# Kernel tuning notes

Measured on AMD Instinct MI355X. Metric: run time of the kernel, lower is better.

The kernel has to match this reference:

```python
import jax, jax.numpy as jnp
import numpy as np

LN_EPS = 1e-5


def _ln(x, g, b):
    m = jnp.mean(x, axis=-1, keepdims=True)
    v = jnp.mean((x - m) ** 2, axis=-1, keepdims=True)
    return (x - m) / jnp.sqrt(v + LN_EPS) * g + b


def setup_inputs() -> dict:
    key = jax.random.key(0)
    ks = jax.random.split(key, 8)
    B, N, S, D, T = 16, 64, 2048, 1024, 768

    def xavier(k, shape):
        fan_in, fan_out = shape
        lim = (6.0 / (fan_in + fan_out)) ** 0.5
        return jax.random.uniform(k, shape, minval=-lim, maxval=lim, dtype=jnp.float32)

    return {
        "prev_states": jax.random.normal(ks[0], (B, N, D), dtype=jnp.float32),
        "input_tokens": jax.random.normal(ks[1], (B, S, T), dtype=jnp.float32),
        # input_projection (token_dim -> state_dim)
        "W_proj": xavier(ks[2], (T, D)),
        "b_proj": jnp.zeros((D,), jnp.float32),
        # three LayerNorms
        "g_state": jnp.ones((D,), jnp.float32), "beta_state": jnp.zeros((D,), jnp.float32),
        "g_input": jnp.ones((D,), jnp.float32), "beta_input": jnp.zeros((D,), jnp.float32),
        "g_out": jnp.ones((D,), jnp.float32), "beta_out": jnp.zeros((D,), jnp.float32),
        # GRU gates (2D -> D); update-gate bias initialized to -1 as in the module
        "W_u": xavier(ks[3], (2 * D, D)), "b_u": jnp.full((D,), -1.0, jnp.float32),
        "W_r": xavier(ks[4], (2 * D, D)), "b_r": jnp.zeros((D,), jnp.float32),
        "W_n": xavier(ks[5], (2 * D, D)), "b_n": jnp.zeros((D,), jnp.float32),
    }


def reference(prev_states, input_tokens, W_proj, b_proj,
              g_state, beta_state, g_input, beta_input, g_out, beta_out,
              W_u, b_u, W_r, b_r, W_n, b_n):
    D = prev_states.shape[-1]
    # project tokens to state dim: (B,S,D)
    tok = input_tokens @ W_proj + b_proj
    # attention routing (routing_weights=None path)
    scores = jnp.einsum('bnd,bsd->bns', prev_states, tok) / jnp.sqrt(jnp.float32(D))
    attn = jax.nn.softmax(scores, axis=-1)
    routed = jnp.einsum('bns,bsd->bnd', attn, tok)  # (B,N,D)
    # GRU-style gated update, vectorized over the num_states axis
    ps_n = _ln(prev_states, g_state, beta_state)
    in_n = _ln(routed, g_input, beta_input)
    concat = jnp.concatenate([ps_n, in_n], axis=-1)  # (B,N,2D)
    u = jax.nn.sigmoid(concat @ W_u + b_u)
    r = jax.nn.sigmoid(concat @ W_r + b_r)
    reset_in = jnp.concatenate([r * ps_n, in_n], axis=-1)
    cand = jnp.tanh(reset_in @ W_n + b_n)  # dropout is identity in eval
    new_state = (1.0 - u) * prev_states + u * cand
    return _ln(new_state, g_out, beta_out)
```

## Files before the change

kernel.cpp:

```cpp
#include <hip/hip_runtime.h>
#include <stdint.h>

typedef __attribute__((ext_vector_type(4))) float floatx4;
typedef __attribute__((ext_vector_type(8))) short shortx8;

#define LN_EPS 1e-5f

__device__ __forceinline__ unsigned short f2b(float f) {
  unsigned u = __builtin_bit_cast(unsigned, f);
  u = (u + 0x7FFFu + ((u >> 16) & 1u)) >> 16;
  return (unsigned short)u;
}
__device__ __forceinline__ float b2f(unsigned short h) {
  return __builtin_bit_cast(float, (unsigned)h << 16);
}

__device__ __forceinline__ void g2l16(const unsigned short* g, unsigned short* l) {
  __builtin_amdgcn_global_load_lds(
      (const __attribute__((address_space(1))) unsigned int*)g,
      (__attribute__((address_space(3))) unsigned int*)l, 16, 0, 0);
}

__device__ __forceinline__ float wave_sum(float v) {
#pragma unroll
  for (int o = 32; o; o >>= 1) v += __shfl_down(v, o, 64);
  return v;
}
__device__ __forceinline__ float block_sum(float v, float* s) {
  v = wave_sum(v);
  __syncthreads();
  if ((threadIdx.x & 63) == 0) s[threadIdx.x >> 6] = v;
  __syncthreads();
  return s[0] + s[1] + s[2] + s[3];
}

__global__ __launch_bounds__(256) void k_transpose_to_bf16(
    const float* __restrict__ in, unsigned short* __restrict__ out, int K, int N) {
  __shared__ float tile[32][33];
  const int k0 = blockIdx.x * 32, n0 = blockIdx.y * 32;
  const int tx = threadIdx.x & 31, ty = threadIdx.x >> 5;
#pragma unroll
  for (int i = 0; i < 32; i += 8)
    tile[ty + i][tx] = in[(long)(k0 + ty + i) * N + n0 + tx];
  __syncthreads();
#pragma unroll
  for (int i = 0; i < 32; i += 8)
    out[(long)(n0 + ty + i) * K + k0 + tx] = f2b(tile[tx][ty + i]);
}

__global__ __launch_bounds__(256) void k_transpose3(
    const float* __restrict__ Wu, const float* __restrict__ Wr,
    const float* __restrict__ Wn, unsigned short* __restrict__ Wtur,
    unsigned short* __restrict__ Wtn) {
  __shared__ float tile[32][33];
  const int which = blockIdx.z;
  const float* in = which == 0 ? Wu : (which == 1 ? Wr : Wn);
  unsigned short* out = which == 0 ? Wtur : (which == 1 ? Wtur + 1024 * 2048 : Wtn);
  const int K = 2048, N = 1024;
  const int k0 = blockIdx.x * 32, n0 = blockIdx.y * 32;
  const int tx = threadIdx.x & 31, ty = threadIdx.x >> 5;
#pragma unroll
  for (int i = 0; i < 32; i += 8)
    tile[ty + i][tx] = in[(long)(k0 + ty + i) * N + n0 + tx];
  __syncthreads();
#pragma unroll
  for (int i = 0; i < 32; i += 8)
    out[(long)(n0 + ty + i) * K + k0 + tx] = f2b(tile[tx][ty + i]);
}

__global__ __launch_bounds__(256) void k_cvt3(
    const float* __restrict__ prev, unsigned short* __restrict__ psb,
    const float* __restrict__ toks, unsigned short* __restrict__ tokb,
    const float* __restrict__ wp, unsigned short* __restrict__ wpb) {
  const long chunk = (long)blockIdx.x * 256 + threadIdx.x;
  const float* src;
  unsigned short* dst;
  long i;
  if (chunk < 262144) { src = prev; dst = psb; i = chunk * 4; }
  else if (chunk < 6553600) { src = toks; dst = tokb; i = (chunk - 262144) * 4; }
  else { src = wp; dst = wpb; i = (chunk - 6553600) * 4; }
  floatx4 v = *(const floatx4*)(src + i);
  unsigned short t4[4];
#pragma unroll
  for (int j = 0; j < 4; j++) t4[j] = f2b(v[j]);
  *(uint2*)(dst + i) = *(uint2*)t4;
}

__global__ __launch_bounds__(256) void k_gemm64(
    const unsigned short* __restrict__ A, long sAb, long sAk, int lda,
    const unsigned short* __restrict__ Bt, long sBb, long sBk, int ldb,
    int K, int nsplit,
    const float* __restrict__ bias, const float* __restrict__ bias2,
    float scale, int mode,
    void* __restrict__ out, int ldc, long sCb, long sCk,
    unsigned short* __restrict__ out2,
    const unsigned short* __restrict__ aux_psn,
    const float* __restrict__ aux_u, const float* __restrict__ aux_prev) {
  __shared__ unsigned short As[64 * 64];
  __shared__ unsigned short Bs[64 * 64];
  const int tid = threadIdx.x;
  const int wave = tid >> 6, lane = tid & 63;
  const int z = blockIdx.z;
  const int b = (nsplit == 2) ? (z >> 1) : z;
  const int kc = (nsplit == 2) ? (z & 1) : 0;
  const int m0 = blockIdx.x * 64, n0 = blockIdx.y * 64;
  const int wm = wave & 1, wn = wave >> 1;
  const int l16 = lane & 15, quad = lane >> 4;
  const int srow8 = lane >> 3;
  const int c8 = ((lane & 7) ^ srow8) * 8;
  const unsigned short* Ab = A + (long)b * sAb + (long)kc * sAk;
  const unsigned short* Bb = Bt + (long)b * sBb + (long)kc * sBk;

  const unsigned short* gA[2];
  const unsigned short* gB[2];
  unsigned short* lA[2];
  unsigned short* lB[2];
#pragma unroll
  for (int j = 0; j < 2; j++) {
    const int rb = wave * 16 + j * 8;
    gA[j] = Ab + (long)(m0 + rb + srow8) * lda + c8;
    gB[j] = Bb + (long)(n0 + rb + srow8) * ldb + c8;
    lA[j] = &As[rb * 64];
    lB[j] = &Bs[rb * 64];
  }
  int offA[2][2], offB[2][2];
#pragma unroll
  for (int ks = 0; ks < 2; ks++)
#pragma unroll
    for (int i = 0; i < 2; i++) {
      int r = wm * 32 + i * 16 + l16;
      offA[ks][i] = r * 64 + (((ks * 4 + quad) ^ (r & 7)) * 8);
      r = wn * 32 + i * 16 + l16;
      offB[ks][i] = r * 64 + (((ks * 4 + quad) ^ (r & 7)) * 8);
    }

  floatx4 acc[2][2] = {};

  for (int k0 = 0; k0 < K; k0 += 64) {
#pragma unroll
    for (int j = 0; j < 2; j++) {
      g2l16(gA[j] + k0, lA[j]);
      g2l16(gB[j] + k0, lB[j]);
    }
    __syncthreads();
#pragma unroll
    for (int ks = 0; ks < 2; ks++) {
      shortx8 af[2], bf[2];
#pragma unroll
      for (int i = 0; i < 2; i++) af[i] = *(const shortx8*)&As[offA[ks][i]];
#pragma unroll
      for (int j = 0; j < 2; j++) bf[j] = *(const shortx8*)&Bs[offB[ks][j]];
#pragma unroll
      for (int i = 0; i < 2; i++)
#pragma unroll
        for (int j = 0; j < 2; j++)
          acc[i][j] = __builtin_amdgcn_mfma_f32_16x16x32_bf16(af[i], bf[j], acc[i][j], 0, 0, 0);
    }
    __syncthreads();
  }

#pragma unroll
  for (int i = 0; i < 2; i++)
#pragma unroll
    for (int j = 0; j < 2; j++) {
      const int rbase = m0 + wm * 32 + i * 16 + quad * 4;
      const int c = n0 + wn * 32 + j * 16 + l16;
      float bval = 0.0f;
      if (bias) bval = (mode == 5 && c >= 1024) ? bias2[c - 1024] : bias[c];
#pragma unroll
      for (int r = 0; r < 4; r++) {
        const int row = rbase + r;
        float v = acc[i][j][r] * scale + bval;
        const long cidx = (long)b * sCb + (long)kc * sCk + (long)row * ldc + c;
        if (mode == 0) {
          out2[cidx] = f2b(expf(v));
        } else if (mode == 1) {
          out2[cidx] = f2b(v);
        } else if (mode == 3) {
          float cand = tanhf(v);
          float u = aux_u[(long)row * 1024 + c];
          float p = aux_prev[(long)row * 1024 + c];
          ((float*)out)[cidx] = (1.0f - u) * p + u * cand;
        } else if (mode == 6) {
          ((float*)out)[cidx] = v + aux_u[row] * bias2[c];
        } else {
          if (c < 1024) {
            ((float*)out)[(long)row * 1024 + c] = 1.0f / (1.0f + expf(-v));
          } else {
            const int cc = c - 1024;
            float rr = 1.0f / (1.0f + expf(-v));
            out2[(long)row * 2048 + cc] = f2b(rr * b2f(aux_psn[(long)row * 2048 + cc]));
          }
        }
      }
    }
}

__global__ __launch_bounds__(256) void k_routed_mfma(
    const unsigned short* __restrict__ attnb,
    const unsigned short* __restrict__ tok,
    float* __restrict__ parts) {
  __shared__ unsigned short As[64 * 40];
  __shared__ unsigned short Bs[32 * 66];
  const int kc = blockIdx.x, nt = blockIdx.y, b = blockIdx.z;
  const int tid = threadIdx.x;
  const int wave = tid >> 6, lane = tid & 63;
  const int wm = wave & 1, wn = wave >> 1;
  const int l16 = lane & 15, quad = lane >> 4;
  const int n0 = nt * 64;
  const long abase = (long)b * 131072 + (long)kc * 1024;
  const long tbase = ((long)b * 2048 + (long)kc * 1024) * 768;
  const int srow = tid >> 2, skc = (tid & 3) * 8;
  const int bk = tid >> 3, bd = (tid & 7) * 8;

  floatx4 acc[2][2] = {};

  for (int k0 = 0; k0 < 1024; k0 += 32) {
    *(uint4*)&As[srow * 40 + skc] =
        *(const uint4*)(attnb + abase + (long)srow * 2048 + k0 + skc);
    {
      uint4 v = *(const uint4*)(tok + tbase + (long)(k0 + bk) * 768 + n0 + bd);
      const unsigned* pv = (const unsigned*)&v;
      unsigned short* dst = &Bs[bk * 66 + bd];
#pragma unroll
      for (int w2 = 0; w2 < 4; w2++) *(unsigned*)(dst + w2 * 2) = pv[w2];
    }
    __syncthreads();

    shortx8 a0 = *(const shortx8*)&As[(wm * 32 + 0  + l16) * 40 + quad * 8];
    shortx8 a1 = *(const shortx8*)&As[(wm * 32 + 16 + l16) * 40 + quad * 8];
    shortx8 b0, b1;
#pragma unroll
    for (int j = 0; j < 8; j++) {
      b0[j] = *(const short*)&Bs[(quad * 8 + j) * 66 + wn * 32 + l16];
      b1[j] = *(const short*)&Bs[(quad * 8 + j) * 66 + wn * 32 + 16 + l16];
    }
    acc[0][0] = __builtin_amdgcn_mfma_f32_16x16x32_bf16(a0, b0, acc[0][0], 0, 0, 0);
    acc[0][1] = __builtin_amdgcn_mfma_f32_16x16x32_bf16(a0, b1, acc[0][1], 0, 0, 0);
    acc[1][0] = __builtin_amdgcn_mfma_f32_16x16x32_bf16(a1, b0, acc[1][0], 0, 0, 0);
    acc[1][1] = __builtin_amdgcn_mfma_f32_16x16x32_bf16(a1, b1, acc[1][1], 0, 0, 0);
    __syncthreads();
  }

#pragma unroll
  for (int im = 0; im < 2; im++)
#pragma unroll
    for (int in_ = 0; in_ < 2; in_++) {
      const int rbase = wm * 32 + im * 16 + quad * 4;
      const int c = n0 + wn * 32 + in_ * 16 + l16;
#pragma unroll
      for (int r = 0; r < 4; r++)
        parts[(long)kc * 786432 + ((long)b * 64 + rbase + r) * 768 + c] =
            acc[im][in_][r];
    }
}

__global__ __launch_bounds__(256) void k_rowsum(
    const unsigned short* __restrict__ w, float* __restrict__ rs) {
  __shared__ float scr[4];
  const long r = blockIdx.x;
  const int t = threadIdx.x;
  uint4 v = *(const uint4*)(w + r * 2048 + t * 8);
  const unsigned short* h = (const unsigned short*)&v;
  float s = 0.0f;
#pragma unroll
  for (int i = 0; i < 8; i++) s += b2f(h[i]);
  s = block_sum(s, scr);
  if (t == 0) rs[r] = s;
}

__global__ __launch_bounds__(256) void k_sumcvt(
    const float* __restrict__ parts, unsigned short* __restrict__ out) {
  const long i = ((long)blockIdx.x * 256 + threadIdx.x) * 4;
  floatx4 v = *(const floatx4*)(parts + i);
  floatx4 w = *(const floatx4*)(parts + 786432 + i);
  unsigned short t4[4];
#pragma unroll
  for (int j = 0; j < 4; j++) t4[j] = f2b(v[j] + w[j]);
  *(uint2*)(out + i) = *(uint2*)t4;
}

__global__ __launch_bounds__(256) void k_ln2(
    const float* __restrict__ prev, const float* __restrict__ routed,
    const float* __restrict__ g_st, const float* __restrict__ be_st,
    const float* __restrict__ g_in, const float* __restrict__ be_in,
    unsigned short* __restrict__ conc, unsigned short* __restrict__ candA) {
  __shared__ float scr[4];
  const long r = blockIdx.x & 1023;
  const bool second = blockIdx.x >= 1024;
  const int t = threadIdx.x;
  floatx4 v;
  const float *g, *be;
  if (!second) {
    v = *(const floatx4*)(prev + r * 1024 + t * 4);
    g = g_st; be = be_st;
  } else {
    v = *(const floatx4*)(routed + r * 1024 + t * 4);
    g = g_in; be = be_in;
  }
  float s1 = v[0] + v[1] + v[2] + v[3];
  float s2 = v[0] * v[0] + v[1] * v[1] + v[2] * v[2] + v[3] * v[3];
  s1 = block_sum(s1, scr);
  s2 = block_sum(s2, scr);
  const float mean = s1 * (1.0f / 1024.0f);
  const float var = s2 * (1.0f / 1024.0f) - mean * mean;
  const float rstd = rsqrtf(var + LN_EPS);
#pragma unroll
  for (int i = 0; i < 4; i++) {
    const int d = t * 4 + i;
    const float y = (v[i] - mean) * rstd * g[d] + be[d];
    const unsigned short h = f2b(y);
    if (!second) {
      conc[r * 2048 + d] = h;
    } else {
      conc[r * 2048 + 1024 + d] = h;
      candA[r * 2048 + 1024 + d] = h;
    }
  }
}

__global__ __launch_bounds__(256) void k_ln_out(
    const float* __restrict__ in, const float* __restrict__ g,
    const float* __restrict__ be, float* __restrict__ out) {
  __shared__ float scr[4];
  const long r = blockIdx.x;
  const int t = threadIdx.x;
  floatx4 v = *(const floatx4*)(in + r * 1024 + t * 4);
  float s1 = v[0] + v[1] + v[2] + v[3];
  float s2 = v[0] * v[0] + v[1] * v[1] + v[2] * v[2] + v[3] * v[3];
  s1 = block_sum(s1, scr);
  s2 = block_sum(s2, scr);
  const float mean = s1 * (1.0f / 1024.0f);
  const float var = s2 * (1.0f / 1024.0f) - mean * mean;
  const float rstd = rsqrtf(var + LN_EPS);
  floatx4 o;
#pragma unroll
  for (int i = 0; i < 4; i++) {
    const int d = t * 4 + i;
    o[i] = (v[i] - mean) * rstd * g[d] + be[d];
  }
  *(floatx4*)(out + r * 1024 + t * 4) = o;
}

extern "C" void kernel_launch(void* const* d_in, const int* in_sizes, int n_in,
                              void* d_out, int out_size, void* d_ws, size_t ws_size,
                              hipStream_t stream) {
  (void)in_sizes; (void)n_in; (void)out_size; (void)ws_size;
  const float* prev  = (const float*)d_in[0];
  const float* toks  = (const float*)d_in[1];
  const float* Wp    = (const float*)d_in[2];
  const float* bp    = (const float*)d_in[3];
  const float* g_st  = (const float*)d_in[4];
  const float* be_st = (const float*)d_in[5];
  const float* g_in  = (const float*)d_in[6];
  const float* be_in = (const float*)d_in[7];
  const float* g_o   = (const float*)d_in[8];
  const float* be_o  = (const float*)d_in[9];
  const float* Wu    = (const float*)d_in[10];
  const float* bu    = (const float*)d_in[11];
  const float* Wr    = (const float*)d_in[12];
  const float* br    = (const float*)d_in[13];
  const float* Wn    = (const float*)d_in[14];
  const float* bn    = (const float*)d_in[15];
  float* out = (float*)d_out;

  char* ws = (char*)d_ws;
  unsigned short* tokb  = (unsigned short*)ws; ws += 50331648;
  unsigned short* psb   = (unsigned short*)ws; ws += 2097152;
  unsigned short* Wpb   = (unsigned short*)ws; ws += 1572864;
  unsigned short* Wtp   = (unsigned short*)ws; ws += 1572864;
  unsigned short* pwb   = (unsigned short*)ws; ws += 1572864;
  unsigned short* attnb = (unsigned short*)ws; ws += 4194304;
  float*          rowsum= (float*)ws;          ws += 4096;
  float*          parts = (float*)ws;          ws += 6291456;
  unsigned short* rwb   = (unsigned short*)ws; ws += 1572864;
  float*          routed= (float*)ws;          ws += 4194304;
  unsigned short* conc  = (unsigned short*)ws; ws += 4194304;
  unsigned short* candA = (unsigned short*)ws; ws += 4194304;
  float*          ubuf  = (float*)ws;          ws += 4194304;
  float*          ns    = (float*)ws;          ws += 4194304;
  unsigned short* Wtur  = (unsigned short*)ws; ws += 8388608;
  unsigned short* Wtn   = (unsigned short*)ws; ws += 4194304;

  const dim3 blk(256);

  k_cvt3<<<dim3(26368), blk, 0, stream>>>(prev, psb, toks, tokb, Wp, Wpb);
  k_transpose_to_bf16<<<dim3(24, 32), blk, 0, stream>>>(Wp, Wtp, 768, 1024);
  k_transpose3<<<dim3(64, 32, 3), blk, 0, stream>>>(Wu, Wr, Wn, Wtur, Wtn);
  k_gemm64<<<dim3(16, 12, 1), blk, 0, stream>>>(
      psb, 0L, 0L, 1024, Wpb, 0L, 0L, 1024, 1024, 1,
      nullptr, nullptr, 1.0f, 1,
      nullptr, 768, 0L, 0L, pwb, nullptr, nullptr, nullptr);
  k_gemm64<<<dim3(1, 32, 16), blk, 0, stream>>>(
      pwb, 49152L, 0L, 768, tokb, 1572864L, 0L, 768, 768, 1,
      nullptr, nullptr, 0.03125f, 0,
      nullptr, 2048, 131072L, 0L, attnb, nullptr, nullptr, nullptr);
  k_rowsum<<<dim3(1024), blk, 0, stream>>>(attnb, rowsum);
  k_routed_mfma<<<dim3(2, 12, 16), blk, 0, stream>>>(attnb, tokb, parts);
  k_sumcvt<<<dim3(768), blk, 0, stream>>>(parts, rwb);
  k_gemm64<<<dim3(16, 16, 1), blk, 0, stream>>>(
      rwb, 0L, 0L, 768, Wtp, 0L, 0L, 768, 768, 1,
      nullptr, bp, 1.0f, 6,
      (void*)routed, 1024, 0L, 0L, nullptr, nullptr, rowsum, nullptr);
  k_ln2<<<dim3(2048), blk, 0, stream>>>(prev, routed, g_st, be_st, g_in, be_in,
                                        conc, candA);
  k_gemm64<<<dim3(16, 32, 1), blk, 0, stream>>>(
      conc, 0L, 0L, 2048, Wtur, 0L, 0L, 2048, 2048, 1,
      bu, br, 1.0f, 5,
      (void*)ubuf, 1024, 0L, 0L, candA, conc, nullptr, nullptr);
  k_gemm64<<<dim3(16, 16, 1), blk, 0, stream>>>(
      candA, 0L, 0L, 2048, Wtn, 0L, 0L, 2048, 2048, 1,
      bn, nullptr, 1.0f, 3,
      (void*)ns, 1024, 0L, 0L, nullptr, nullptr, ubuf, prev);
  k_ln_out<<<dim3(1024), blk, 0, stream>>>(ns, g_o, be_o, out);
}
```

Baseline: 340.8 us.

## Double-buffer GEMM tiles, fuse softmax rowsum into score GEMM, merge transposes

The main GEMM now double-buffers its LDS tiles, so the next K-tile's global-to-LDS load is issued before the current tile's MFMAs. The score GEMM computes softmax row sums in its epilogue through shuffles and atomicAdd into a buffer that k_cvt3 zeroes, which removes the k_rowsum kernel. The routed kernel prefetches the next A/B tiles into registers and replaces __syncthreads with lighter barriers. The Wp transpose is merged with the three GRU weight transposes into one launch. Together these cut launches and hide memory latency, at the cost of doubled LDS use, atomics, and rowsums now taken from fp32 values rather than the rounded bf16 ones.

```diff
diff --git a/kernel.cpp b/kernel.cpp
--- a/kernel.cpp
+++ b/kernel.cpp
@@ -34,10 +34,23 @@
   return s[0] + s[1] + s[2] + s[3];
 }
 
-__global__ __launch_bounds__(256) void k_transpose_to_bf16(
-    const float* __restrict__ in, unsigned short* __restrict__ out, int K, int N) {
+__global__ __launch_bounds__(256) void k_transpose4(
+    const float* __restrict__ Wu, const float* __restrict__ Wr,
+    const float* __restrict__ Wn, const float* __restrict__ Wp,
+    unsigned short* __restrict__ Wtur, unsigned short* __restrict__ Wtn,
+    unsigned short* __restrict__ Wtp) {
   __shared__ float tile[32][33];
+  const int which = blockIdx.z;
+  const float* in;
+  unsigned short* out;
+  int K;
+  if (which == 0)      { in = Wu; out = Wtur;              K = 2048; }
+  else if (which == 1) { in = Wr; out = Wtur + 1024 * 2048; K = 2048; }
+  else if (which == 2) { in = Wn; out = Wtn;               K = 2048; }
+  else                 { in = Wp; out = Wtp;               K = 768;  }
+  const int N = 1024;
   const int k0 = blockIdx.x * 32, n0 = blockIdx.y * 32;
+  if (k0 >= K) return;
   const int tx = threadIdx.x & 31, ty = threadIdx.x >> 5;
 #pragma unroll
   for (int i = 0; i < 32; i += 8)
@@ -48,30 +61,15 @@
     out[(long)(n0 + ty + i) * K + k0 + tx] = f2b(tile[tx][ty + i]);
 }
 
-__global__ __launch_bounds__(256) void k_transpose3(
-    const float* __restrict__ Wu, const float* __restrict__ Wr,
-    const float* __restrict__ Wn, unsigned short* __restrict__ Wtur,
-    unsigned short* __restrict__ Wtn) {
-  __shared__ float tile[32][33];
-  const int which = blockIdx.z;
-  const float* in = which == 0 ? Wu : (which == 1 ? Wr : Wn);
-  unsigned short* out = which == 0 ? Wtur : (which == 1 ? Wtur + 1024 * 2048 : Wtn);
-  const int K = 2048, N = 1024;
-  const int k0 = blockIdx.x * 32, n0 = blockIdx.y * 32;
-  const int tx = threadIdx.x & 31, ty = threadIdx.x >> 5;
-#pragma unroll
-  for (int i = 0; i < 32; i += 8)
-    tile[ty + i][tx] = in[(long)(k0 + ty + i) * N + n0 + tx];
-  __syncthreads();
-#pragma unroll
-  for (int i = 0; i < 32; i += 8)
-    out[(long)(n0 + ty + i) * K + k0 + tx] = f2b(tile[tx][ty + i]);
-}
-
 __global__ __launch_bounds__(256) void k_cvt3(
     const float* __restrict__ prev, unsigned short* __restrict__ psb,
     const float* __restrict__ toks, unsigned short* __restrict__ tokb,
-    const float* __restrict__ wp, unsigned short* __restrict__ wpb) {
+    const float* __restrict__ wp, unsigned short* __restrict__ wpb,
+    float* __restrict__ rs) {
+  if (blockIdx.x == 0) {
+    floatx4 z = {0.f, 0.f, 0.f, 0.f};
+    *(floatx4*)(rs + threadIdx.x * 4) = z;
+  }
   const long chunk = (long)blockIdx.x * 256 + threadIdx.x;
   const float* src;
   unsigned short* dst;
@@ -87,41 +85,39 @@
 }
 
 __global__ __launch_bounds__(256) void k_gemm64(
-    const unsigned short* __restrict__ A, long sAb, long sAk, int lda,
-    const unsigned short* __restrict__ Bt, long sBb, long sBk, int ldb,
-    int K, int nsplit,
+    const unsigned short* __restrict__ A, long sAb, int lda,
+    const unsigned short* __restrict__ Bt, long sBb, int ldb,
+    int K,
     const float* __restrict__ bias, const float* __restrict__ bias2,
     float scale, int mode,
-    void* __restrict__ out, int ldc, long sCb, long sCk,
+    void* __restrict__ out, int ldc, long sCb,
     unsigned short* __restrict__ out2,
     const unsigned short* __restrict__ aux_psn,
-    const float* __restrict__ aux_u, const float* __restrict__ aux_prev) {
-  __shared__ unsigned short As[64 * 64];
-  __shared__ unsigned short Bs[64 * 64];
+    const float* __restrict__ aux_u, const float* __restrict__ aux_prev,
+    float* __restrict__ rs) {
+  __shared__ unsigned short As[2][64 * 64];
+  __shared__ unsigned short Bs[2][64 * 64];
   const int tid = threadIdx.x;
   const int wave = tid >> 6, lane = tid & 63;
-  const int z = blockIdx.z;
-  const int b = (nsplit == 2) ? (z >> 1) : z;
-  const int kc = (nsplit == 2) ? (z & 1) : 0;
+  const int b = blockIdx.z;
   const int m0 = blockIdx.x * 64, n0 = blockIdx.y * 64;
   const int wm = wave & 1, wn = wave >> 1;
   const int l16 = lane & 15, quad = lane >> 4;
   const int srow8 = lane >> 3;
   const int c8 = ((lane & 7) ^ srow8) * 8;
-  const unsigned short* Ab = A + (long)b * sAb + (long)kc * sAk;
-  const unsigned short* Bb = Bt + (long)b * sBb + (long)kc * sBk;
+  const unsigned short* Ab = A + (long)b * sAb;
+  const unsigned short* Bb = Bt + (long)b * sBb;
 
   const unsigned short* gA[2];
   const unsigned short* gB[2];
-  unsigned short* lA[2];
-  unsigned short* lB[2];
+  int lAoff[2], lBoff[2];
 #pragma unroll
   for (int j = 0; j < 2; j++) {
     const int rb = wave * 16 + j * 8;
     gA[j] = Ab + (long)(m0 + rb + srow8) * lda + c8;
     gB[j] = Bb + (long)(n0 + rb + srow8) * ldb + c8;
-    lA[j] = &As[rb * 64];
-    lB[j] = &Bs[rb * 64];
+    lAoff[j] = rb * 64;
+    lBoff[j] = rb * 64;
   }
   int offA[2][2], offB[2][2];
 #pragma unroll
@@ -136,20 +132,31 @@
 
   floatx4 acc[2][2] = {};
 
-  for (int k0 = 0; k0 < K; k0 += 64) {
-#pragma unroll
-    for (int j = 0; j < 2; j++) {
-      g2l16(gA[j] + k0, lA[j]);
-      g2l16(gB[j] + k0, lB[j]);
-    }
-    __syncthreads();
+#pragma unroll
+  for (int j = 0; j < 2; j++) {
+    g2l16(gA[j], &As[0][lAoff[j]]);
+    g2l16(gB[j], &Bs[0][lBoff[j]]);
+  }
+  __syncthreads();
+
+  const int nt = K >> 6;
+  for (int t = 0; t < nt; t++) {
+    const int cur = t & 1;
+    if (t + 1 < nt) {
+      const int kn = (t + 1) << 6;
+#pragma unroll
+      for (int j = 0; j < 2; j++) {
+        g2l16(gA[j] + kn, &As[cur ^ 1][lAoff[j]]);
+        g2l16(gB[j] + kn, &Bs[cur ^ 1][lBoff[j]]);
+      }
+    }
 #pragma unroll
     for (int ks = 0; ks < 2; ks++) {
       shortx8 af[2], bf[2];
 #pragma unroll
-      for (int i = 0; i < 2; i++) af[i] = *(const shortx8*)&As[offA[ks][i]];
-#pragma unroll
-      for (int j = 0; j < 2; j++) bf[j] = *(const shortx8*)&Bs[offB[ks][j]];
+      for (int i = 0; i < 2; i++) af[i] = *(const shortx8*)&As[cur][offA[ks][i]];
+#pragma unroll
+      for (int j = 0; j < 2; j++) bf[j] = *(const shortx8*)&Bs[cur][offB[ks][j]];
 #pragma unroll
       for (int i = 0; i < 2; i++)
 #pragma unroll
@@ -157,6 +164,35 @@
           acc[i][j] = __builtin_amdgcn_mfma_f32_16x16x32_bf16(af[i], bf[j], acc[i][j], 0, 0, 0);
     }
     __syncthreads();
+  }
+
+  if (mode == 0) {
+#pragma unroll
+    for (int i = 0; i < 2; i++) {
+      float psum[4] = {0.f, 0.f, 0.f, 0.f};
+#pragma unroll
+      for (int j = 0; j < 2; j++) {
+        const int rbase = m0 + wm * 32 + i * 16 + quad * 4;
+        const int c = n0 + wn * 32 + j * 16 + l16;
+#pragma unroll
+        for (int r = 0; r < 4; r++) {
+          const float e = expf(acc[i][j][r] * scale);
+          out2[(long)b * sCb + (long)(rbase + r) * ldc + c] = f2b(e);
+          psum[r] += e;
+        }
+      }
+#pragma unroll
+      for (int r = 0; r < 4; r++) {
+        float s = psum[r];
+        s += __shfl_xor(s, 1, 64);
+        s += __shfl_xor(s, 2, 64);
+        s += __shfl_xor(s, 4, 64);
+        s += __shfl_xor(s, 8, 64);
+        if (l16 == 0)
+          atomicAdd(rs + (long)b * 64 + m0 + wm * 32 + i * 16 + quad * 4 + r, s);
+      }
+    }
+    return;
   }
 
 #pragma unroll
@@ -171,10 +207,8 @@
       for (int r = 0; r < 4; r++) {
         const int row = rbase + r;
         float v = acc[i][j][r] * scale + bval;
-        const long cidx = (long)b * sCb + (long)kc * sCk + (long)row * ldc + c;
-        if (mode == 0) {
-          out2[cidx] = f2b(expf(v));
-        } else if (mode == 1) {
+        const long cidx = (long)b * sCb + (long)row * ldc + c;
+        if (mode == 1) {
           out2[cidx] = f2b(v);
         } else if (mode == 3) {
           float cand = tanhf(v);
@@ -215,17 +249,24 @@
 
   floatx4 acc[2][2] = {};
 
+  uint4 pa = *(const uint4*)(attnb + abase + (long)srow * 2048 + skc);
+  uint4 pb = *(const uint4*)(tok + tbase + (long)bk * 768 + n0 + bd);
+
   for (int k0 = 0; k0 < 1024; k0 += 32) {
-    *(uint4*)&As[srow * 40 + skc] =
-        *(const uint4*)(attnb + abase + (long)srow * 2048 + k0 + skc);
+    *(uint4*)&As[srow * 40 + skc] = pa;
     {
-      uint4 v = *(const uint4*)(tok + tbase + (long)(k0 + bk) * 768 + n0 + bd);
-      const unsigned* pv = (const unsigned*)&v;
+      const unsigned* pv = (const unsigned*)&pb;
       unsigned short* dst = &Bs[bk * 66 + bd];
 #pragma unroll
       for (int w2 = 0; w2 < 4; w2++) *(unsigned*)(dst + w2 * 2) = pv[w2];
     }
-    __syncthreads();
+    if (k0 + 32 < 1024) {
+      pa = *(const uint4*)(attnb + abase + (long)srow * 2048 + (k0 + 32) + skc);
+      pb = *(const uint4*)(tok + tbase + (long)(k0 + 32 + bk) * 768 + n0 + bd);
+    }
+    asm volatile("s_waitcnt lgkmcnt(0)" ::: "memory");
+    __builtin_amdgcn_s_barrier();
+    __builtin_amdgcn_sched_barrier(0);
 
     shortx8 a0 = *(const shortx8*)&As[(wm * 32 + 0  + l16) * 40 + quad * 8];
     shortx8 a1 = *(const shortx8*)&As[(wm * 32 + 16 + l16) * 40 + quad * 8];
@@ -239,7 +280,7 @@
     acc[0][1] = __builtin_amdgcn_mfma_f32_16x16x32_bf16(a0, b1, acc[0][1], 0, 0, 0);
     acc[1][0] = __builtin_amdgcn_mfma_f32_16x16x32_bf16(a1, b0, acc[1][0], 0, 0, 0);
     acc[1][1] = __builtin_amdgcn_mfma_f32_16x16x32_bf16(a1, b1, acc[1][1], 0, 0, 0);
-    __syncthreads();
+    __builtin_amdgcn_s_barrier();
   }
 
 #pragma unroll
@@ -253,20 +294,6 @@
         parts[(long)kc * 786432 + ((long)b * 64 + rbase + r) * 768 + c] =
             acc[im][in_][r];
     }
-}
-
-__global__ __launch_bounds__(256) void k_rowsum(
-    const unsigned short* __restrict__ w, float* __restrict__ rs) {
-  __shared__ float scr[4];
-  const long r = blockIdx.x;
-  const int t = threadIdx.x;
-  uint4 v = *(const uint4*)(w + r * 2048 + t * 8);
-  const unsigned short* h = (const unsigned short*)&v;
-  float s = 0.0f;
-#pragma unroll
-  for (int i = 0; i < 8; i++) s += b2f(h[i]);
-  s = block_sum(s, scr);
-  if (t == 0) rs[r] = s;
 }
 
 __global__ __launch_bounds__(256) void k_sumcvt(
@@ -384,33 +411,31 @@
 
   const dim3 blk(256);
 
-  k_cvt3<<<dim3(26368), blk, 0, stream>>>(prev, psb, toks, tokb, Wp, Wpb);
-  k_transpose_to_bf16<<<dim3(24, 32), blk, 0, stream>>>(Wp, Wtp, 768, 1024);
-  k_transpose3<<<dim3(64, 32, 3), blk, 0, stream>>>(Wu, Wr, Wn, Wtur, Wtn);
+  k_cvt3<<<dim3(26368), blk, 0, stream>>>(prev, psb, toks, tokb, Wp, Wpb, rowsum);
+  k_transpose4<<<dim3(64, 32, 4), blk, 0, stream>>>(Wu, Wr, Wn, Wp, Wtur, Wtn, Wtp);
   k_gemm64<<<dim3(16, 12, 1), blk, 0, stream>>>(
-      psb, 0L, 0L, 1024, Wpb, 0L, 0L, 1024, 1024, 1,
+      psb, 0L, 1024, Wpb, 0L, 1024, 1024,
       nullptr, nullptr, 1.0f, 1,
-      nullptr, 768, 0L, 0L, pwb, nullptr, nullptr, nullptr);
+      nullptr, 768, 0L, pwb, nullptr, nullptr, nullptr, nullptr);
   k_gemm64<<<dim3(1, 32, 16), blk, 0, stream>>>(
-      pwb, 49152L, 0L, 768, tokb, 1572864L, 0L, 768, 768, 1,
+      pwb, 49152L, 768, tokb, 1572864L, 768, 768,
       nullptr, nullptr, 0.03125f, 0,
-      nullptr, 2048, 131072L, 0L, attnb, nullptr, nullptr, nullptr);
-  k_rowsum<<<dim3(1024), blk, 0, stream>>>(attnb, rowsum);
+      nullptr, 2048, 131072L, attnb, nullptr, nullptr, nullptr, rowsum);
   k_routed_mfma<<<dim3(2, 12, 16), blk, 0, stream>>>(attnb, tokb, parts);
   k_sumcvt<<<dim3(768), blk, 0, stream>>>(parts, rwb);
   k_gemm64<<<dim3(16, 16, 1), blk, 0, stream>>>(
-      rwb, 0L, 0L, 768, Wtp, 0L, 0L, 768, 768, 1,
+      rwb, 0L, 768, Wtp, 0L, 768, 768,
       nullptr, bp, 1.0f, 6,
-      (void*)routed, 1024, 0L, 0L, nullptr, nullptr, rowsum, nullptr);
+      (void*)routed, 1024, 0L, nullptr, nullptr, rowsum, nullptr, nullptr);
   k_ln2<<<dim3(2048), blk, 0, stream>>>(prev, routed, g_st, be_st, g_in, be_in,
                                         conc, candA);
   k_gemm64<<<dim3(16, 32, 1), blk, 0, stream>>>(
-      conc, 0L, 0L, 2048, Wtur, 0L, 0L, 2048, 2048, 1,
+      conc, 0L, 2048, Wtur, 0L, 2048, 2048,
       bu, br, 1.0f, 5,
-      (void*)ubuf, 1024, 0L, 0L, candA, conc, nullptr, nullptr);
+      (void*)ubuf, 1024, 0L, candA, conc, nullptr, nullptr, nullptr);
   k_gemm64<<<dim3(16, 16, 1), blk, 0, stream>>>(
-      candA, 0L, 0L, 2048, Wtn, 0L, 0L, 2048, 2048, 1,
+      candA, 0L, 2048, Wtn, 0L, 2048, 2048,
       bn, nullptr, 1.0f, 3,
-      (void*)ns, 1024, 0L, 0L, nullptr, nullptr, ubuf, prev);
+      (void*)ns, 1024, 0L, nullptr, nullptr, ubuf, prev, nullptr);
   k_ln_out<<<dim3(1024), blk, 0, stream>>>(ns, g_o, be_o, out);
 }
```

Result: faster. 330.9 us (-2.9%).
